# Performance work log

Measured on AMD Instinct MI355X. Metric: run time of the kernel, lower is better.

The kernel has to match this reference:

```python
import jax, jax.numpy as jnp
import numpy as np

B = 16        # graphs per protein batch
NPG = 2000    # nodes per graph
N = B * NPG   # total nodes
E = 640000    # total edges
H, C = 3, 128 # heads, hidden_dim
FIN = 1038
K = 400       # ceil(0.2 * NPG) SAGPool keep count
NEG = 0.1     # LeakyReLU slope in model
EPS = 1e-5


def setup_inputs() -> dict:
    key = jax.random.key(0)
    ks = jax.random.split(key, 24)
    d = {}
    d['p1_x'] = jax.random.normal(ks[0], (N, FIN), jnp.float32)
    d['p2_x'] = jax.random.normal(ks[1], (N, FIN), jnp.float32)
    d['p1_edge_index'] = jax.random.randint(ks[2], (2, E), 0, N, jnp.int32)
    d['p2_edge_index'] = jax.random.randint(ks[3], (2, E), 0, N, jnp.int32)
    d['p1_edge_attr'] = jax.random.uniform(ks[4], (E, 2), jnp.float32)
    d['p2_edge_attr'] = jax.random.uniform(ks[5], (E, 2), jnp.float32)
    s_in = 1.0 / np.sqrt(FIN)
    s_h = 1.0 / np.sqrt(C)
    # GATv2Conv params (lin_l has bias, lin_r no bias, lin_edge, att, out bias)
    d['Wl'] = jax.random.normal(ks[6], (FIN, H * C), jnp.float32) * s_in
    d['bl'] = jnp.zeros((H * C,), jnp.float32)
    d['Wr'] = jax.random.normal(ks[7], (FIN, H * C), jnp.float32) * s_in
    d['We'] = jax.random.normal(ks[8], (2, H * C), jnp.float32) * 0.5
    d['att'] = jax.random.normal(ks[9], (H, C), jnp.float32) * s_h
    d['conv_bias'] = jnp.zeros((C,), jnp.float32)
    # BatchNorm1d
    d['gamma'] = jnp.ones((C,), jnp.float32)
    d['beta'] = jnp.zeros((C,), jnp.float32)
    # SAGPooling scorer: GraphConv(C -> 1)
    d['gc_Wrel'] = jax.random.normal(ks[10], (C, 1), jnp.float32) * s_h
    d['gc_Wroot'] = jax.random.normal(ks[11], (C, 1), jnp.float32) * s_h
    d['gc_b'] = jnp.zeros((1,), jnp.float32)
    # MLP head
    d['W1'] = jax.random.normal(ks[12], (2 * C, C), jnp.float32) / np.sqrt(2 * C)
    d['b1'] = jnp.zeros((C,), jnp.float32)
    d['W2'] = jax.random.normal(ks[13], (C, C // 2), jnp.float32) * s_h
    d['b2'] = jnp.zeros((C // 2,), jnp.float32)
    d['Wo'] = jax.random.normal(ks[14], (C // 2, 1), jnp.float32) / np.sqrt(C // 2)
    d['bo'] = jnp.zeros((1,), jnp.float32)
    return d


def gatv2(x, ei, ea, Wl, bl, Wr, We, att, conv_bias):
    # GATv2Conv, heads=3, concat=False, edge_dim=2, add_self_loops (fill='mean')
    loop = jnp.arange(N, dtype=ei.dtype)
    src = jnp.concatenate([ei[0], loop])
    dst = jnp.concatenate([ei[1], loop])
    ea_full = jnp.concatenate([ea, jnp.broadcast_to(ea.mean(0), (N, ea.shape[1]))], 0)
    xl = (x @ Wl + bl).reshape(N, H, C)
    xr = (x @ Wr).reshape(N, H, C)
    ef = (ea_full @ We).reshape(-1, H, C)
    m = xl[src] + xr[dst] + ef                      # [E+N, H, C]
    e = jnp.einsum('ehc,hc->eh', jax.nn.leaky_relu(m, 0.2), att)
    emax = jax.ops.segment_max(e, dst, num_segments=N)
    ex = jnp.exp(e - emax[dst])
    denom = jax.ops.segment_sum(ex, dst, num_segments=N)
    alpha = ex / denom[dst]                          # softmax per dst node, per head
    out = jax.ops.segment_sum(alpha[:, :, None] * xl[src], dst, num_segments=N)
    return out.mean(1) + conv_bias                   # concat=False -> head mean


def branch(x, ei, ea, Wl, bl, Wr, We, att, conv_bias, gamma, beta,
           gc_Wrel, gc_Wroot, gc_b):
    h = gatv2(x, ei, ea, Wl, bl, Wr, We, att, conv_bias)
    h = jax.nn.leaky_relu(h, NEG)
    mu = h.mean(0)
    var = ((h - mu) ** 2).mean(0)
    h = (h - mu) / jnp.sqrt(var + EPS) * gamma + beta  # BatchNorm1d (batch stats)
    # SAGPooling scorer: GraphConv out_i = W_root x_i + W_rel sum_{j->i} x_j + b
    agg = jax.ops.segment_sum(h[ei[0]], ei[1], num_segments=N)
    score = jnp.tanh((h @ gc_Wroot + agg @ gc_Wrel + gc_b)[:, 0])  # [N]
    s = score.reshape(B, NPG)
    topv, topi = jax.lax.top_k(s, K)                 # per-graph top-k
    hb = h.reshape(B, NPG, C)
    hsel = jnp.take_along_axis(hb, topi[:, :, None], axis=1)  # [B, K, C]
    hsel = hsel * topv[:, :, None]                   # x[perm] * tanh(score)[perm]
    return hsel.mean(1)                              # global mean pool -> [B, C]


def reference(p1_x, p2_x, p1_edge_attr, p2_edge_attr, Wl, bl, Wr, We, att,
              conv_bias, gamma, beta, gc_Wrel, gc_Wroot, gc_b, W1, b1, W2, b2,
              Wo, bo, p1_edge_index, p2_edge_index):
    x1 = branch(p1_x, p1_edge_index, p1_edge_attr, Wl, bl, Wr, We, att,
                conv_bias, gamma, beta, gc_Wrel, gc_Wroot, gc_b)
    x2 = branch(p2_x, p2_edge_index, p2_edge_attr, Wl, bl, Wr, We, att,
                conv_bias, gamma, beta, gc_Wrel, gc_Wroot, gc_b)
    xc = jnp.concatenate([x1, x2], 1)                # [B, 2C]
    xc = jax.nn.leaky_relu(xc @ W1 + b1, NEG)
    xc = jax.nn.leaky_relu(xc @ W2 + b2, NEG)
    return jax.nn.sigmoid(xc @ Wo + bo)              # [B, 1]
```

## Files before the change

### kernel.cpp

```cpp
#include <hip/hip_runtime.h>
#include <hip/hip_bf16.h>
#include <math.h>

#define NN 32000
#define EE 640000
#define CC 128
#define HC 384
#define FIN 1038
#define KP 1056
#define KT 33
#define BB 16
#define NPG 2000
#define KK 400

#define XLR_STR 12288000u
#define HBN_STR 4096000u
#define OFF_STR 32064u

#define XL_OFF     0u
#define XR_OFF     24576000u
#define HBN_OFF    49152000u
#define SSRC_OFF   57344000u
#define SEA_OFF    58624000u
#define CNT_OFF    61184000u
#define BNSUM_OFF  61248000u
#define BNSQ_OFF   61248256u
#define MEANEA_OFF 61248512u
#define ZERO_BYTES ((61248516u - 61184000u) * 4u)
#define OFFS_OFF   61248576u
#define CUR_OFF    61312704u
#define R_OFF      61376704u
#define REL_OFF    61440704u
#define SCORE_OFF  61504704u
#define XB_OFF     61568704u
#define WTH_OFF    61572800u

typedef __attribute__((ext_vector_type(8))) _Float16 f16x8;
typedef __attribute__((ext_vector_type(2))) _Float16 f16x2;
typedef __attribute__((ext_vector_type(4))) float f32x4;
typedef __attribute__((ext_vector_type(8))) unsigned short us8;

typedef const __attribute__((address_space(1))) unsigned int* gp1_t;
typedef __attribute__((address_space(3))) unsigned int* lp3_t;
__device__ __forceinline__ void gl_lds16(const void* g, void* l) {
    __builtin_amdgcn_global_load_lds((gp1_t)g, (lp3_t)l, 16, 0, 0);
}

__global__ __launch_bounds__(256) void k_prep(const int* __restrict__ ei0, const int* __restrict__ ei1,
                                              const float* __restrict__ ea0, const float* __restrict__ ea1,
                                              int* __restrict__ cnt, float* __restrict__ meanea) {
    int b = blockIdx.x;
    int br = (b >= 2500);
    int tid = threadIdx.x;
    int e = (b - br * 2500) * 256 + tid;
    const int* ei = br ? ei1 : ei0;
    const float* ea = br ? ea1 : ea0;
    cnt += br * NN; meanea += br * 2;
    float s0 = 0.f, s1 = 0.f;
    if (e < EE) {
        atomicAdd(&cnt[ei[EE + e]], 1);
        float2 t = ((const float2*)ea)[e];
        s0 = t.x; s1 = t.y;
    }
    __shared__ float r0[256], r1[256];
    r0[tid] = s0; r1[tid] = s1; __syncthreads();
    for (int st = 128; st; st >>= 1) {
        if (tid < st) { r0[tid] += r0[tid + st]; r1[tid] += r1[tid + st]; }
        __syncthreads();
    }
    if (tid == 0) { atomicAdd(&meanea[0], r0[0]); atomicAdd(&meanea[1], r1[0]); }
}

__global__ __launch_bounds__(1024) void k_scan(const int* __restrict__ cnt, int* __restrict__ offs, int* __restrict__ cur) {
    int br = blockIdx.x;
    cnt += br * NN; offs += br * OFF_STR; cur += br * NN;
    __shared__ int sb[1024];
    int tid = threadIdx.x;
    int base = tid * 32;
    int s = 0;
    for (int i = 0; i < 32; i++) { int idx = base + i; s += (idx < NN) ? cnt[idx] : 0; }
    sb[tid] = s; __syncthreads();
    for (int off = 1; off < 1024; off <<= 1) {
        int v = (tid >= off) ? sb[tid - off] : 0;
        __syncthreads();
        sb[tid] += v;
        __syncthreads();
    }
    int run = sb[tid] - s;
    for (int i = 0; i < 32; i++) {
        int idx = base + i;
        if (idx < NN) { int c = cnt[idx]; offs[idx] = run; cur[idx] = run; run += c; }
    }
    if (tid == 1023) offs[NN] = run;
}

__global__ __launch_bounds__(256) void k_scatter(const int* __restrict__ ei0, const int* __restrict__ ei1,
                                                 const float* __restrict__ ea0, const float* __restrict__ ea1,
                                                 int* __restrict__ cur, int2* __restrict__ sed) {
    int b = blockIdx.x;
    int br = (b >= 2500);
    int e = (b - br * 2500) * 256 + threadIdx.x;
    const int* ei = br ? ei1 : ei0;
    const float* ea = br ? ea1 : ea0;
    cur += br * NN; sed += br * EE;
    if (e < EE) {
        int d = ei[EE + e];
        int p = atomicAdd(&cur[d], 1);
        float2 t = ((const float2*)ea)[e];
        f16x2 h; h[0] = (_Float16)t.x; h[1] = (_Float16)t.y;
        int2 pk;
        pk.x = ei[e];
        pk.y = __builtin_bit_cast(int, h);
        sed[p] = pk;
    }
}

__global__ __launch_bounds__(256) void k_cvtW(const float* __restrict__ Wl_, const float* __restrict__ Wr_,
                                              unsigned short* __restrict__ Bh) {
    int idx = blockIdx.x * 256 + threadIdx.x;
    if (idx >= 768 * (KP / 8)) return;
    int n = idx / (KP / 8);
    int seg = idx - n * (KP / 8);
    int c0 = seg * 8;
    const float* W = (n < HC) ? Wl_ : Wr_;
    int nc = (n < HC) ? n : n - HC;
    us8 h8;
#pragma unroll
    for (int j = 0; j < 8; ++j) {
        int k = c0 + j;
        float v = (k < FIN) ? W[(size_t)k * HC + nc] : 0.f;
        _Float16 h = (_Float16)v;
        h8[j] = __builtin_bit_cast(unsigned short, h);
    }
    *(us8*)&Bh[(size_t)n * KP + c0] = h8;
}

__global__ __launch_bounds__(256) void k_gemm2f(const float* __restrict__ x0, const float* __restrict__ x1,
                                                const unsigned short* __restrict__ Bh,
                                                const float* __restrict__ bias, float* __restrict__ ws) {
    __shared__ _Float16 sA[2][128 * 32], sB[2][128 * 32];
    const int bid = blockIdx.x;
    const int br = (bid >= 1504);
    const int b2 = br ? (bid - 1504) : bid;
    const float* x = br ? x1 : x0;
    _Float16* xlh = (_Float16*)(ws + XL_OFF) + (size_t)br * XLR_STR;
    float* xr = ws + XR_OFF + br * XLR_STR;

    const int xcd = b2 & 7, slot = b2 >> 3;
    const int t = xcd * 188 + slot;
    if (t >= 1500) return;
    const int mt = t / 6, nt = t - mt * 6;
    const int bm = mt * 128, bn = nt * 128;

    const int tid = threadIdx.x;
    const int wave = tid >> 6, lane = tid & 63;
    const int wm = (wave >> 1) * 64, wn = (wave & 1) * 64;
    const int quad = lane >> 4, l15 = lane & 15;

    const int srow = wave * 16 + (lane >> 2);
    const int scol = (lane & 3) * 8;
    const size_t gB0 = (size_t)(bn + srow) * KP + scol;
    const size_t gB1 = (size_t)(bn + 64 + srow) * KP + scol;
    const int lB0 = (wave * 16) * 32 + lane * 8;
    const int lB1 = (64 + wave * 16) * 32 + lane * 8;

    const int arow0 = wave * 32 + (lane >> 2);
    const int acol = (lane & 3) * 8;

    float af[2][8];

#define LOADA(KT_) do {                                                         \
        int gcol = (KT_) * 32 + acol;                                           \
        if (gcol >= FIN) gcol = 0;                                              \
        _Pragma("unroll")                                                       \
        for (int rep = 0; rep < 2; ++rep) {                                     \
            const float* gp = x + (size_t)(bm + arow0 + rep * 16) * FIN + gcol; \
            float2 v01 = ((const float2*)gp)[0];                                \
            float2 v23 = ((const float2*)gp)[1];                                \
            float2 v45 = ((const float2*)gp)[2];                                \
            float2 v67 = ((const float2*)gp)[3];                                \
            af[rep][0] = v01.x; af[rep][1] = v01.y;                             \
            af[rep][2] = v23.x; af[rep][3] = v23.y;                             \
            af[rep][4] = v45.x; af[rep][5] = v45.y;                             \
            af[rep][6] = v67.x; af[rep][7] = v67.y;                             \
        } } while (0)

#define CVTWRITE(BUF_) do {                                                     \
        _Pragma("unroll")                                                       \
        for (int rep = 0; rep < 2; ++rep) {                                     \
            f16x8 a;                                                            \
            _Pragma("unroll")                                                   \
            for (int j = 0; j < 8; ++j) a[j] = (_Float16)af[rep][j];            \
            *(f16x8*)&sA[BUF_][(arow0 + rep * 16) * 32 + acol] = a;             \
        } } while (0)

    f32x4 acc[4][4];
#pragma unroll
    for (int i = 0; i < 4; ++i)
#pragma unroll
        for (int j = 0; j < 4; ++j) {
            f32x4 z = {0.f, 0.f, 0.f, 0.f};
            acc[i][j] = z;
        }

    const int aoff0 = (wm + l15) * 32 + quad * 8;
    const int boff0 = (wn + l15) * 32 + quad * 8;

    gl_lds16(Bh + gB0, &sB[0][lB0]);
    gl_lds16(Bh + gB1, &sB[0][lB1]);
    LOADA(0);
    CVTWRITE(0);
    __syncthreads();

    for (int kt = 0; kt < KT; ++kt) {
        const int cur = kt & 1, nxt = cur ^ 1;
        const bool pf = (kt + 1 < KT);
        if (pf) {
            const int kc = (kt + 1) * 32;
            gl_lds16(Bh + gB0 + kc, &sB[nxt][lB0]);
            gl_lds16(Bh + gB1 + kc, &sB[nxt][lB1]);
            LOADA(kt + 1);
        }
        f16x8 bfr[4];
#pragma unroll
        for (int j = 0; j < 4; ++j) bfr[j] = *(const f16x8*)&sB[cur][boff0 + j * 512];
#pragma unroll
        for (int i = 0; i < 4; ++i) {
            f16x8 a = *(const f16x8*)&sA[cur][aoff0 + i * 512];
#pragma unroll
            for (int j = 0; j < 4; ++j)
                acc[i][j] = __builtin_amdgcn_mfma_f32_16x16x32_f16(a, bfr[j], acc[i][j], 0, 0, 0);
        }
        if (pf) CVTWRITE(nxt);
        __syncthreads();
    }
#undef LOADA
#undef CVTWRITE

    const bool isL = (nt < 3);
    if (isL) {
#pragma unroll
        for (int j = 0; j < 4; ++j) {
            const int ncol = wn + j * 16 + l15;
            const float bj = bias[bn + ncol];
#pragma unroll
            for (int i = 0; i < 4; ++i) {
#pragma unroll
                for (int r = 0; r < 4; ++r) {
                    int m = bm + wm + i * 16 + quad * 4 + r;
                    xlh[(size_t)m * HC + bn + ncol] = (_Float16)(acc[i][j][r] + bj);
                }
            }
        }
    } else {
        const int nbase = bn - HC;
#pragma unroll
        for (int j = 0; j < 4; ++j) {
            const int ncol = wn + j * 16 + l15;
#pragma unroll
            for (int i = 0; i < 4; ++i) {
#pragma unroll
                for (int r = 0; r < 4; ++r) {
                    int m = bm + wm + i * 16 + quad * 4 + r;
                    xr[(size_t)m * HC + nbase + ncol] = acc[i][j][r];
                }
            }
        }
    }
}

__global__ __launch_bounds__(256) void k_gat(const unsigned short* __restrict__ xlhb, const float* __restrict__ xrb,
                                             const int* __restrict__ offsb, const int2* __restrict__ sedb,
                                             const float* __restrict__ meaneab,
                                             const float* __restrict__ We, const float* __restrict__ att,
                                             const float* __restrict__ conv_bias, float* __restrict__ houtb) {
    int gwave = (blockIdx.x * 256 + threadIdx.x) >> 6;
    int lane = threadIdx.x & 63;
    int half = lane >> 5, l32 = lane & 31;
    int br = (gwave >= NN);
    int node = gwave - br * NN;
    const _Float16* xlh = (const _Float16*)xlhb + (size_t)br * XLR_STR;
    const float* xr = xrb + br * XLR_STR;
    const int* offs = offsb + br * OFF_STR;
    const int2* sed = sedb + br * EE;
    const float* meanea = meaneab + br * 2;
    float* hout = houtb + br * HBN_STR;

    f16x2 we0p[6], we1p[6], attp[6], xrp[6];
    const float2* xrw = (const float2*)(xr + (size_t)node * HC);
#pragma unroll
    for (int jj = 0; jj < 6; ++jj) {
        int q = l32 + 32 * jj;
        float2 w0 = ((const float2*)We)[q];
        float2 w1 = ((const float2*)(We + HC))[q];
        float2 av = ((const float2*)att)[q];
        float2 xv = xrw[q];
        we0p[jj][0] = (_Float16)w0.x; we0p[jj][1] = (_Float16)w0.y;
        we1p[jj][0] = (_Float16)w1.x; we1p[jj][1] = (_Float16)w1.y;
        attp[jj][0] = (_Float16)av.x; attp[jj][1] = (_Float16)av.y;
        xrp[jj][0]  = (_Float16)xv.x; xrp[jj][1]  = (_Float16)xv.y;
    }
    _Float16 meh0 = (_Float16)(meanea[0] * (1.0f / EE));
    _Float16 meh1 = (_Float16)(meanea[1] * (1.0f / EE));

    int p0 = offs[node], p1 = offs[node + 1];
    int cntE = p1 - p0;
    int iters = (cntE + 2) >> 1;

    float den0 = 0.f, den1 = 0.f, den2 = 0.f;
    float accv[12];
#pragma unroll
    for (int k = 0; k < 12; ++k) accv[k] = 0.f;

    const f16x2 zero2 = {(_Float16)0.f, (_Float16)0.f};
    const f16x2 c02 = {(_Float16)0.2f, (_Float16)0.2f};

    for (int i = 0; i < iters; ++i) {
        int t = 2 * i + half;
        bool self = (t == 0);
        bool valid = (t <= cntE);
        int p = p0 + t - 1;
        if (p < p0) p = p0;
        if (p > EE - 1) p = EE - 1;
        int2 pk = sed[p];
        f16x2 eh = __builtin_bit_cast(f16x2, pk.y);
        int s = self ? node : pk.x;
        _Float16 e0 = self ? meh0 : eh[0];
        _Float16 e1 = self ? meh1 : eh[1];
        f16x2 e0p, e1p;
        e0p[0] = e0; e0p[1] = e0;
        e1p[0] = e1; e1p[1] = e1;

        const f16x2* xrow = (const f16x2*)(xlh + (size_t)s * HC);
        f16x2 xv[6];
#pragma unroll
        for (int jj = 0; jj < 6; ++jj) xv[jj] = xrow[l32 + 32 * jj];

        float pr0 = 0.f, pr1 = 0.f, pr2 = 0.f;
#pragma unroll
        for (int jj = 0; jj < 6; ++jj) {
            f16x2 u = xrp[jj] + e0p * we0p[jj];
            u = u + e1p * we1p[jj];
            f16x2 m = xv[jj] + u;
            f16x2 mx = __builtin_elementwise_max(m, zero2);
            f16x2 mn = __builtin_elementwise_min(m, zero2);
            f16x2 lk = mx + mn * c02;
#if __has_builtin(__builtin_amdgcn_fdot2)
            if (jj < 2)      pr0 = __builtin_amdgcn_fdot2(lk, attp[jj], pr0, false);
            else if (jj < 4) pr1 = __builtin_amdgcn_fdot2(lk, attp[jj], pr1, false);
            else             pr2 = __builtin_amdgcn_fdot2(lk, attp[jj], pr2, false);
#else
            float c = (float)lk[0] * (float)attp[jj][0] + (float)lk[1] * (float)attp[jj][1];
            if (jj < 2) pr0 += c; else if (jj < 4) pr1 += c; else pr2 += c;
#endif
        }
#pragma unroll
        for (int msk = 16; msk; msk >>= 1) {
            pr0 += __shfl_xor(pr0, msk);
            pr1 += __shfl_xor(pr1, msk);
            pr2 += __shfl_xor(pr2, msk);
        }
        float w0 = valid ? __expf(pr0) : 0.f;
        float w1 = valid ? __expf(pr1) : 0.f;
        float w2 = valid ? __expf(pr2) : 0.f;
        den0 += w0; den1 += w1; den2 += w2;
#pragma unroll
        for (int jj = 0; jj < 6; ++jj) {
            float wh = (jj < 2) ? w0 : ((jj < 4) ? w1 : w2);
            accv[2 * jj]     += wh * (float)xv[jj][0];
            accv[2 * jj + 1] += wh * (float)xv[jj][1];
        }
    }

#pragma unroll
    for (int k = 0; k < 12; ++k) accv[k] += __shfl_xor(accv[k], 32);
    den0 += __shfl_xor(den0, 32);
    den1 += __shfl_xor(den1, 32);
    den2 += __shfl_xor(den2, 32);

    if (half == 0) {
        float i0 = 1.f / den0, i1 = 1.f / den1, i2 = 1.f / den2;
#pragma unroll
        for (int jja = 0; jja < 2; ++jja) {
#pragma unroll
            for (int b = 0; b < 2; ++b) {
                int c = (((jja * 32 + l32) << 1) | b);
                float o = (accv[2 * jja + b] * i0 + accv[2 * (jja + 2) + b] * i1 +
                           accv[2 * (jja + 4) + b] * i2) * (1.f / 3.f) + conv_bias[c];
                o = (o > 0.f) ? o : 0.1f * o;
                hout[(size_t)node * CC + c] = o;
            }
        }
    }
}

__global__ __launch_bounds__(256) void k_bnstats(const float* __restrict__ hb, float* __restrict__ bnsumb, float* __restrict__ bnsqb) {
    int b = blockIdx.x;
    int br = b >> 9, lb = b & 511;
    const float* h = hb + br * HBN_STR;
    float* bnsum = bnsumb + br * CC;
    float* bnsq = bnsqb + br * CC;
    int c = threadIdx.x & 127;
    int row0 = lb * 2 + (threadIdx.x >> 7);
    float s = 0.f, ss = 0.f;
    for (int n = row0; n < NN; n += 1024) {
        float v = h[(size_t)n * CC + c];
        s += v; ss += v * v;
    }
    atomicAdd(&bnsum[c], s);
    atomicAdd(&bnsq[c], ss);
}

__global__ __launch_bounds__(256) void k_bnapply(float* __restrict__ hb, const float* __restrict__ bnsumb,
                                                 const float* __restrict__ bnsqb,
                                                 const float* __restrict__ gamma, const float* __restrict__ beta,
                                                 const float* __restrict__ wroot,
                                                 const float* __restrict__ wrel, float* __restrict__ r_b, float* __restrict__ rel_b) {
    int gwave = (blockIdx.x * 256 + threadIdx.x) >> 6;
    int lane = threadIdx.x & 63;
    int br = (gwave >= NN);
    int wave = gwave - br * NN;
    float* h = hb + br * HBN_STR;
    const float* bnsum = bnsumb + br * CC;
    const float* bnsq = bnsqb + br * CC;
    float* r_ = r_b + br * NN;
    float* rel_ = rel_b + br * NN;

    float mu0 = bnsum[lane] * (1.f / NN);
    float var0 = bnsq[lane] * (1.f / NN) - mu0 * mu0;
    float sc0 = gamma[lane] * rsqrtf(var0 + 1e-5f);
    float sh0 = beta[lane] - mu0 * sc0;
    float mu1 = bnsum[64 + lane] * (1.f / NN);
    float var1 = bnsq[64 + lane] * (1.f / NN) - mu1 * mu1;
    float sc1 = gamma[64 + lane] * rsqrtf(var1 + 1e-5f);
    float sh1 = beta[64 + lane] - mu1 * sc1;

    size_t base = (size_t)wave * CC;
    float v0 = h[base + lane], v1 = h[base + 64 + lane];
    v0 = v0 * sc0 + sh0;
    v1 = v1 * sc1 + sh1;
    h[base + lane] = v0;
    h[base + 64 + lane] = v1;
    float pr = v0 * wroot[lane] + v1 * wroot[64 + lane];
    float pl = v0 * wrel[lane] + v1 * wrel[64 + lane];
#pragma unroll
    for (int m = 32; m; m >>= 1) {
        pr += __shfl_xor(pr, m);
        pl += __shfl_xor(pl, m);
    }
    if (lane == 0) { r_[wave] = pr; rel_[wave] = pl; }
}

__global__ __launch_bounds__(256) void k_score(const float* __restrict__ r_b, const float* __restrict__ rel_b,
                                               const int* __restrict__ offsb, const int2* __restrict__ sedb,
                                               const float* __restrict__ gcb, float* __restrict__ scoreb) {
    int gwave = (blockIdx.x * 256 + threadIdx.x) >> 6;
    int lane = threadIdx.x & 63;
    int br = (gwave >= NN);
    int wave = gwave - br * NN;
    const float* r_ = r_b + br * NN;
    const float* rel_ = rel_b + br * NN;
    const int* offs = offsb + br * OFF_STR;
    const int2* sed = sedb + br * EE;
    float* score = scoreb + br * NN;
    int p0 = offs[wave], p1 = offs[wave + 1];
    float s = 0.f;
    for (int p = p0 + lane; p < p1; p += 64) s += rel_[sed[p].x];
#pragma unroll
    for (int m = 32; m; m >>= 1) s += __shfl_xor(s, m);
    if (lane == 0) score[wave] = tanhf(r_[wave] + s + gcb[0]);
}

__global__ __launch_bounds__(1024) void k_topk(const float* __restrict__ scoreb, const float* __restrict__ hb,
                                               float* __restrict__ xbout) {
    __shared__ float sv[2048];
    __shared__ int si[2048];
    __shared__ float red[8][128];
    int b = blockIdx.x, tid = threadIdx.x;
    int br = b >> 4, g = b & 15;
    const float* score = scoreb + br * NN;
    const float* h = hb + br * HBN_STR;
    for (int i = tid; i < 2048; i += 1024) {
        sv[i] = (i < NPG) ? score[g * NPG + i] : -2.0f;
        si[i] = i;
    }
    __syncthreads();
    for (int k = 2; k <= 2048; k <<= 1) {
        for (int j = k >> 1; j > 0; j >>= 1) {
            for (int t = tid; t < 2048; t += 1024) {
                int ixj = t ^ j;
                if (ixj > t) {
                    bool up = ((t & k) == 0);
                    float a = sv[t], bv = sv[ixj];
                    bool sw = up ? (a < bv) : (a > bv);
                    if (sw) {
                        sv[t] = bv; sv[ixj] = a;
                        int tmp = si[t]; si[t] = si[ixj]; si[ixj] = tmp;
                    }
                }
            }
            __syncthreads();
        }
    }
    int grp = tid >> 7, c = tid & 127;
    float a = 0.f;
    for (int kk = grp; kk < KK; kk += 8) {
        int node = g * NPG + si[kk];
        a += sv[kk] * h[(size_t)node * CC + c];
    }
    red[grp][c] = a;
    __syncthreads();
    if (tid < 128) {
        float v = (red[0][tid] + red[1][tid] + red[2][tid] + red[3][tid] +
                   red[4][tid] + red[5][tid] + red[6][tid] + red[7][tid]) * (1.f / KK);
        xbout[(br * BB + g) * CC + tid] = v;
    }
}

__global__ __launch_bounds__(128) void k_mlp(const float* __restrict__ xb, const float* __restrict__ W1,
                                             const float* __restrict__ b1, const float* __restrict__ W2,
                                             const float* __restrict__ b2, const float* __restrict__ Wo,
                                             const float* __restrict__ bo, float* __restrict__ out) {
    int g = blockIdx.x, tid = threadIdx.x;
    __shared__ float xc[256], l1[128], l2[64];
    xc[tid] = xb[g * CC + tid];
    xc[128 + tid] = xb[BB * CC + g * CC + tid];
    __syncthreads();
    float s = b1[tid];
    for (int i = 0; i < 256; i++) s += xc[i] * W1[i * 128 + tid];
    l1[tid] = (s > 0.f) ? s : 0.1f * s;
    __syncthreads();
    if (tid < 64) {
        float s2 = b2[tid];
        for (int i = 0; i < 128; i++) s2 += l1[i] * W2[i * 64 + tid];
        l2[tid] = (s2 > 0.f) ? s2 : 0.1f * s2;
    }
    __syncthreads();
    if (tid < 64) {
        float p = l2[tid] * Wo[tid];
#pragma unroll
        for (int m = 32; m; m >>= 1) p += __shfl_xor(p, m);
        if (tid == 0) out[g] = 1.f / (1.f + __expf(-(p + bo[0])));
    }
}

extern "C" void kernel_launch(void* const* d_in, const int* in_sizes, int n_in,
                              void* d_out, int out_size, void* d_ws, size_t ws_size,
                              hipStream_t stream) {
    (void)in_sizes; (void)n_in; (void)out_size; (void)ws_size;
    const float* x0   = (const float*)d_in[0];
    const float* x1   = (const float*)d_in[1];
    const int*   ei0  = (const int*)d_in[2];
    const int*   ei1  = (const int*)d_in[3];
    const float* ea0  = (const float*)d_in[4];
    const float* ea1  = (const float*)d_in[5];
    const float* Wl   = (const float*)d_in[6];
    const float* bl   = (const float*)d_in[7];
    const float* Wr   = (const float*)d_in[8];
    const float* We   = (const float*)d_in[9];
    const float* att  = (const float*)d_in[10];
    const float* cb   = (const float*)d_in[11];
    const float* gam  = (const float*)d_in[12];
    const float* bet  = (const float*)d_in[13];
    const float* wrel = (const float*)d_in[14];
    const float* wroot= (const float*)d_in[15];
    const float* gcb  = (const float*)d_in[16];
    const float* W1   = (const float*)d_in[17];
    const float* b1   = (const float*)d_in[18];
    const float* W2   = (const float*)d_in[19];
    const float* b2   = (const float*)d_in[20];
    const float* Wo   = (const float*)d_in[21];
    const float* bo   = (const float*)d_in[22];

    float* ws = (float*)d_ws;
    float*  hbn   = ws + HBN_OFF;
    int2*   sed   = (int2*)(ws + SEA_OFF);
    int*    cnt   = (int*)(ws + CNT_OFF);
    float*  bnsum = ws + BNSUM_OFF;
    float*  bnsq  = ws + BNSQ_OFF;
    float*  meanea= ws + MEANEA_OFF;
    int*    offs  = (int*)(ws + OFFS_OFF);
    int*    cur   = (int*)(ws + CUR_OFF);
    float*  r_    = ws + R_OFF;
    float*  rel_  = ws + REL_OFF;
    float*  score = ws + SCORE_OFF;
    float*  xb    = ws + XB_OFF;
    unsigned short* Wth = (unsigned short*)(ws + WTH_OFF);
    unsigned short* xlh = (unsigned short*)(ws + XL_OFF);
    float*  xr    = ws + XR_OFF;

    hipMemsetAsync(cnt, 0, ZERO_BYTES, stream);
    k_cvtW<<<(768 * (KP / 8) + 255) / 256, 256, 0, stream>>>(Wl, Wr, Wth);

    k_prep<<<5000, 256, 0, stream>>>(ei0, ei1, ea0, ea1, cnt, meanea);
    k_scan<<<2, 1024, 0, stream>>>(cnt, offs, cur);
    k_scatter<<<5000, 256, 0, stream>>>(ei0, ei1, ea0, ea1, cur, sed);

    k_gemm2f<<<3008, 256, 0, stream>>>(x0, x1, Wth, bl, ws);

    k_gat<<<16000, 256, 0, stream>>>(xlh, xr, offs, sed, meanea, We, att, cb, hbn);

    k_bnstats<<<1024, 256, 0, stream>>>(hbn, bnsum, bnsq);
    k_bnapply<<<16000, 256, 0, stream>>>(hbn, bnsum, bnsq, gam, bet, wroot, wrel, r_, rel_);
    k_score<<<16000, 256, 0, stream>>>(r_, rel_, offs, sed, gcb, score);
    k_topk<<<32, 1024, 0, stream>>>(score, hbn, xb);

    k_mlp<<<BB, 128, 0, stream>>>(xb, W1, b1, W2, b2, Wo, bo, (float*)d_out);
}
```

Before: 1.254 ms.

## Pre-convert inputs to fp16 and stream GEMM A tiles via direct LDS loads

Result: faster. 1.153 ms (-8.0%).

```diff
diff --git a/kernel.cpp b/kernel.cpp
--- a/kernel.cpp
+++ b/kernel.cpp
@@ -13,27 +13,27 @@
 #define NPG 2000
 #define KK 400
 
-#define XLR_STR 12288000u
+#define XLR_H  12288000u
 #define HBN_STR 4096000u
 #define OFF_STR 32064u
 
-#define XL_OFF     0u
-#define XR_OFF     24576000u
-#define HBN_OFF    49152000u
-#define SSRC_OFF   57344000u
-#define SEA_OFF    58624000u
-#define CNT_OFF    61184000u
-#define BNSUM_OFF  61248000u
-#define BNSQ_OFF   61248256u
-#define MEANEA_OFF 61248512u
-#define ZERO_BYTES ((61248516u - 61184000u) * 4u)
-#define OFFS_OFF   61248576u
-#define CUR_OFF    61312704u
-#define R_OFF      61376704u
-#define REL_OFF    61440704u
-#define SCORE_OFF  61504704u
-#define XB_OFF     61568704u
-#define WTH_OFF    61572800u
+#define XH_OFF     0u
+#define XL_OFF     16896000u
+#define XR_OFF     29184000u
+#define HBN_OFF    41472000u
+#define SED_OFF    49664000u
+#define CNT_OFF    52224000u
+#define BNSUM_OFF  52288000u
+#define BNSQ_OFF   52288256u
+#define MEANEA_OFF 52288512u
+#define ZERO_BYTES ((52288516u - 52224000u) * 4u)
+#define OFFS_OFF   52288576u
+#define CUR_OFF    52352704u
+#define R_OFF      52416704u
+#define REL_OFF    52480704u
+#define SCORE_OFF  52544704u
+#define XB_OFF     52608704u
+#define WTH_OFF    52612800u
 
 typedef __attribute__((ext_vector_type(8))) _Float16 f16x8;
 typedef __attribute__((ext_vector_type(2))) _Float16 f16x2;
@@ -135,23 +135,45 @@
     *(us8*)&Bh[(size_t)n * KP + c0] = h8;
 }
 
-__global__ __launch_bounds__(256) void k_gemm2f(const float* __restrict__ x0, const float* __restrict__ x1,
-                                                const unsigned short* __restrict__ Bh,
-                                                const float* __restrict__ bias, float* __restrict__ ws) {
-    __shared__ _Float16 sA[2][128 * 32], sB[2][128 * 32];
-    const int bid = blockIdx.x;
-    const int br = (bid >= 1504);
-    const int b2 = br ? (bid - 1504) : bid;
-    const float* x = br ? x1 : x0;
-    _Float16* xlh = (_Float16*)(ws + XL_OFF) + (size_t)br * XLR_STR;
-    float* xr = ws + XR_OFF + br * XLR_STR;
-
+__global__ __launch_bounds__(256) void k_cvtX(const float* __restrict__ x, _Float16* __restrict__ xh) {
+    int idx = blockIdx.x * 256 + threadIdx.x;
+    if (idx >= NN * (KP / 8)) return;
+    int row = idx / (KP / 8);
+    int c8 = idx - row * (KP / 8);
+    int col = c8 * 8;
+    const float* gp = x + (size_t)row * FIN + col;
+    f16x8 o;
+    if (col + 8 <= FIN) {
+        float2 v01 = ((const float2*)gp)[0];
+        float2 v23 = ((const float2*)gp)[1];
+        float2 v45 = ((const float2*)gp)[2];
+        float2 v67 = ((const float2*)gp)[3];
+        o[0] = (_Float16)v01.x; o[1] = (_Float16)v01.y;
+        o[2] = (_Float16)v23.x; o[3] = (_Float16)v23.y;
+        o[4] = (_Float16)v45.x; o[5] = (_Float16)v45.y;
+        o[6] = (_Float16)v67.x; o[7] = (_Float16)v67.y;
+    } else {
+#pragma unroll
+        for (int j = 0; j < 8; ++j) o[j] = (_Float16)((col + j < FIN) ? gp[j] : 0.f);
+    }
+    *(f16x8*)&xh[(size_t)row * KP + col] = o;
+}
+
+__global__ __launch_bounds__(256) void k_gemm3(const _Float16* __restrict__ xh,
+                                               const unsigned short* __restrict__ Bh,
+                                               const float* __restrict__ bias, int br,
+                                               float* __restrict__ ws) {
+    __shared__ _Float16 sA[128 * 32], sB[128 * 32];
+    const int b2 = blockIdx.x;
     const int xcd = b2 & 7, slot = b2 >> 3;
     const int t = xcd * 188 + slot;
     if (t >= 1500) return;
     const int mt = t / 6, nt = t - mt * 6;
     const int bm = mt * 128, bn = nt * 128;
 
+    _Float16* xlh = (_Float16*)(ws + XL_OFF) + (size_t)br * XLR_H;
+    _Float16* xrh = (_Float16*)(ws + XR_OFF) + (size_t)br * XLR_H;
+
     const int tid = threadIdx.x;
     const int wave = tid >> 6, lane = tid & 63;
     const int wm = (wave >> 1) * 64, wn = (wave & 1) * 64;
@@ -159,40 +181,12 @@
 
     const int srow = wave * 16 + (lane >> 2);
     const int scol = (lane & 3) * 8;
+    const size_t gA0 = (size_t)(bm + srow) * KP + scol;
+    const size_t gA1 = (size_t)(bm + 64 + srow) * KP + scol;
     const size_t gB0 = (size_t)(bn + srow) * KP + scol;
     const size_t gB1 = (size_t)(bn + 64 + srow) * KP + scol;
-    const int lB0 = (wave * 16) * 32 + lane * 8;
-    const int lB1 = (64 + wave * 16) * 32 + lane * 8;
-
-    const int arow0 = wave * 32 + (lane >> 2);
-    const int acol = (lane & 3) * 8;
-
-    float af[2][8];
-
-#define LOADA(KT_) do {                                                         \
-        int gcol = (KT_) * 32 + acol;                                           \
-        if (gcol >= FIN) gcol = 0;                                              \
-        _Pragma("unroll")                                                       \
-        for (int rep = 0; rep < 2; ++rep) {                                     \
-            const float* gp = x + (size_t)(bm + arow0 + rep * 16) * FIN + gcol; \
-            float2 v01 = ((const float2*)gp)[0];                                \
-            float2 v23 = ((const float2*)gp)[1];                                \
-            float2 v45 = ((const float2*)gp)[2];                                \
-            float2 v67 = ((const float2*)gp)[3];                                \
-            af[rep][0] = v01.x; af[rep][1] = v01.y;                             \
-            af[rep][2] = v23.x; af[rep][3] = v23.y;                             \
-            af[rep][4] = v45.x; af[rep][5] = v45.y;                             \
-            af[rep][6] = v67.x; af[rep][7] = v67.y;                             \
-        } } while (0)
-
-#define CVTWRITE(BUF_) do {                                                     \
-        _Pragma("unroll")                                                       \
-        for (int rep = 0; rep < 2; ++rep) {                                     \
-            f16x8 a;                                                            \
-            _Pragma("unroll")                                                   \
-            for (int j = 0; j < 8; ++j) a[j] = (_Float16)af[rep][j];            \
-            *(f16x8*)&sA[BUF_][(arow0 + rep * 16) * 32 + acol] = a;             \
-        } } while (0)
+    const int lds0 = (wave * 16) * 32 + lane * 8;
+    const int lds1 = (64 + wave * 16) * 32 + lane * 8;
 
     f32x4 acc[4][4];
 #pragma unroll
@@ -206,36 +200,25 @@
     const int aoff0 = (wm + l15) * 32 + quad * 8;
     const int boff0 = (wn + l15) * 32 + quad * 8;
 
-    gl_lds16(Bh + gB0, &sB[0][lB0]);
-    gl_lds16(Bh + gB1, &sB[0][lB1]);
-    LOADA(0);
-    CVTWRITE(0);
-    __syncthreads();
-
     for (int kt = 0; kt < KT; ++kt) {
-        const int cur = kt & 1, nxt = cur ^ 1;
-        const bool pf = (kt + 1 < KT);
-        if (pf) {
-            const int kc = (kt + 1) * 32;
-            gl_lds16(Bh + gB0 + kc, &sB[nxt][lB0]);
-            gl_lds16(Bh + gB1 + kc, &sB[nxt][lB1]);
-            LOADA(kt + 1);
-        }
+        const int kc = kt * 32;
+        gl_lds16(xh + gA0 + kc, &sA[lds0]);
+        gl_lds16(xh + gA1 + kc, &sA[lds1]);
+        gl_lds16(Bh + gB0 + kc, &sB[lds0]);
+        gl_lds16(Bh + gB1 + kc, &sB[lds1]);
+        __syncthreads();
         f16x8 bfr[4];
 #pragma unroll
-        for (int j = 0; j < 4; ++j) bfr[j] = *(const f16x8*)&sB[cur][boff0 + j * 512];
+        for (int j = 0; j < 4; ++j) bfr[j] = *(const f16x8*)&sB[boff0 + j * 512];
 #pragma unroll
         for (int i = 0; i < 4; ++i) {
-            f16x8 a = *(const f16x8*)&sA[cur][aoff0 + i * 512];
+            f16x8 a = *(const f16x8*)&sA[aoff0 + i * 512];
 #pragma unroll
             for (int j = 0; j < 4; ++j)
                 acc[i][j] = __builtin_amdgcn_mfma_f32_16x16x32_f16(a, bfr[j], acc[i][j], 0, 0, 0);
         }
-        if (pf) CVTWRITE(nxt);
         __syncthreads();
     }
-#undef LOADA
-#undef CVTWRITE
 
     const bool isL = (nt < 3);
     if (isL) {
@@ -262,14 +245,14 @@
 #pragma unroll
                 for (int r = 0; r < 4; ++r) {
                     int m = bm + wm + i * 16 + quad * 4 + r;
-                    xr[(size_t)m * HC + nbase + ncol] = acc[i][j][r];
+                    xrh[(size_t)m * HC + nbase + ncol] = (_Float16)acc[i][j][r];
                 }
             }
         }
     }
 }
 
-__global__ __launch_bounds__(256) void k_gat(const unsigned short* __restrict__ xlhb, const float* __restrict__ xrb,
+__global__ __launch_bounds__(256) void k_gat(const unsigned short* __restrict__ xlhb, const unsigned short* __restrict__ xrhb,
                                              const int* __restrict__ offsb, const int2* __restrict__ sedb,
                                              const float* __restrict__ meaneab,
                                              const float* __restrict__ We, const float* __restrict__ att,
@@ -279,26 +262,25 @@
     int half = lane >> 5, l32 = lane & 31;
     int br = (gwave >= NN);
     int node = gwave - br * NN;
-    const _Float16* xlh = (const _Float16*)xlhb + (size_t)br * XLR_STR;
-    const float* xr = xrb + br * XLR_STR;
+    const _Float16* xlh = (const _Float16*)xlhb + (size_t)br * XLR_H;
+    const _Float16* xrh = (const _Float16*)xrhb + (size_t)br * XLR_H;
     const int* offs = offsb + br * OFF_STR;
     const int2* sed = sedb + br * EE;
     const float* meanea = meaneab + br * 2;
     float* hout = houtb + br * HBN_STR;
 
     f16x2 we0p[6], we1p[6], attp[6], xrp[6];
-    const float2* xrw = (const float2*)(xr + (size_t)node * HC);
+    const f16x2* xrw = (const f16x2*)(xrh + (size_t)node * HC);
 #pragma unroll
     for (int jj = 0; jj < 6; ++jj) {
         int q = l32 + 32 * jj;
         float2 w0 = ((const float2*)We)[q];
         float2 w1 = ((const float2*)(We + HC))[q];
         float2 av = ((const float2*)att)[q];
-        float2 xv = xrw[q];
         we0p[jj][0] = (_Float16)w0.x; we0p[jj][1] = (_Float16)w0.y;
         we1p[jj][0] = (_Float16)w1.x; we1p[jj][1] = (_Float16)w1.y;
         attp[jj][0] = (_Float16)av.x; attp[jj][1] = (_Float16)av.y;
-        xrp[jj][0]  = (_Float16)xv.x; xrp[jj][1]  = (_Float16)xv.y;
+        xrp[jj] = xrw[q];
     }
     _Float16 meh0 = (_Float16)(meanea[0] * (1.0f / EE));
     _Float16 meh1 = (_Float16)(meanea[1] * (1.0f / EE));
@@ -573,8 +555,11 @@
     const float* bo   = (const float*)d_in[22];
 
     float* ws = (float*)d_ws;
+    _Float16* xh  = (_Float16*)(ws + XH_OFF);
+    unsigned short* xlh = (unsigned short*)(ws + XL_OFF);
+    unsigned short* xrh = (unsigned short*)(ws + XR_OFF);
     float*  hbn   = ws + HBN_OFF;
-    int2*   sed   = (int2*)(ws + SEA_OFF);
+    int2*   sed   = (int2*)(ws + SED_OFF);
     int*    cnt   = (int*)(ws + CNT_OFF);
     float*  bnsum = ws + BNSUM_OFF;
     float*  bnsq  = ws + BNSQ_OFF;
@@ -586,8 +571,6 @@
     float*  score = ws + SCORE_OFF;
     float*  xb    = ws + XB_OFF;
     unsigned short* Wth = (unsigned short*)(ws + WTH_OFF);
-    unsigned short* xlh = (unsigned short*)(ws + XL_OFF);
-    float*  xr    = ws + XR_OFF;
 
     hipMemsetAsync(cnt, 0, ZERO_BYTES, stream);
     k_cvtW<<<(768 * (KP / 8) + 255) / 256, 256, 0, stream>>>(Wl, Wr, Wth);
@@ -596,9 +579,12 @@
     k_scan<<<2, 1024, 0, stream>>>(cnt, offs, cur);
     k_scatter<<<5000, 256, 0, stream>>>(ei0, ei1, ea0, ea1, cur, sed);
 
-    k_gemm2f<<<3008, 256, 0, stream>>>(x0, x1, Wth, bl, ws);
-
-    k_gat<<<16000, 256, 0, stream>>>(xlh, xr, offs, sed, meanea, We, att, cb, hbn);
+    k_cvtX<<<(NN * (KP / 8) + 255) / 256, 256, 0, stream>>>(x0, xh);
+    k_gemm3<<<1504, 256, 0, stream>>>(xh, Wth, bl, 0, ws);
+    k_cvtX<<<(NN * (KP / 8) + 255) / 256, 256, 0, stream>>>(x1, xh);
+    k_gemm3<<<1504, 256, 0, stream>>>(xh, Wth, bl, 1, ws);
+
+    k_gat<<<16000, 256, 0, stream>>>(xlh, xrh, offs, sed, meanea, We, att, cb, hbn);
 
     k_bnstats<<<1024, 256, 0, stream>>>(hbn, bnsum, bnsq);
     k_bnapply<<<16000, 256, 0, stream>>>(hbn, bnsum, bnsq, gam, bet, wroot, wrel, r_, rel_);
```
